# Performance work log

Hardware: AMD Instinct MI355X
Metric: run time of the kernel (lower is better)

Reference implementation:

```python
import jax, jax.numpy as jnp
import numpy as np

TEMP = 0.5
EPS = 1e-12  # matches torch F.normalize default eps


def _l2_normalize(x):
    n = jnp.sqrt(jnp.sum(x * x, axis=1, keepdims=True))
    return x / jnp.maximum(n, EPS)


def setup_inputs() -> dict:
    key = jax.random.key(0)
    k1, k2 = jax.random.split(key)
    B, D = 4096, 256
    return {
        "x_i": jax.random.normal(k1, (B, D), dtype=jnp.float32),
        "x_j": jax.random.normal(k2, (B, D), dtype=jnp.float32),
    }


def reference(x_i, x_j):
    B = x_i.shape[0]
    z = jnp.concatenate([_l2_normalize(x_i), _l2_normalize(x_j)], axis=0)  # [2B, D]
    # cosine similarity of normalized vectors == plain matmul
    sim = z @ z.T  # [2B, 2B]
    pos = jnp.concatenate([jnp.diagonal(sim, B), jnp.diagonal(sim, -B)], axis=0)  # [2B]
    neg_mask = 1.0 - jnp.eye(2 * B, dtype=sim.dtype)
    denom = jnp.sum(neg_mask * jnp.exp(sim / TEMP), axis=1)  # [2B]
    # -log(exp(pos/T) / denom) = -pos/T + log(denom)
    loss = jnp.sum(-(pos / TEMP) + jnp.log(denom)) / (2 * B)
    return loss
```

## Files before the change

kernel.cpp:

```cpp
#include <hip/hip_runtime.h>
#include <hip/hip_bf16.h>

#define B_ROWS 4096
#define NROWS  8192
#define D      256
#define TILES  64
#define NPAIRS 2080

typedef __attribute__((ext_vector_type(8))) short bf16x8;
typedef __attribute__((ext_vector_type(4))) float floatx4;

__device__ __forceinline__ void load16_to_lds(const short* g, short* l) {
    __builtin_amdgcn_global_load_lds(
        (const __attribute__((address_space(1))) unsigned int*)g,
        (__attribute__((address_space(3))) unsigned int*)l,
        16, 0, 0);
}

__global__ __launch_bounds__(256) void norm_pos_kernel(
    const float* __restrict__ xi, const float* __restrict__ xj,
    short* __restrict__ z, float* __restrict__ pos,
    float* __restrict__ selfdot) {
    int p    = blockIdx.x * 4 + (threadIdx.x >> 6);
    int lane = threadIdx.x & 63;
    float4 v1 = ((const float4*)(xi + (size_t)p * D))[lane];
    float4 v2 = ((const float4*)(xj + (size_t)p * D))[lane];
    float ss1 = v1.x * v1.x + v1.y * v1.y + v1.z * v1.z + v1.w * v1.w;
    float ss2 = v2.x * v2.x + v2.y * v2.y + v2.z * v2.z + v2.w * v2.w;
#pragma unroll
    for (int off = 32; off > 0; off >>= 1) {
        ss1 += __shfl_xor(ss1, off);
        ss2 += __shfl_xor(ss2, off);
    }
    float sc1 = 1.0f / fmaxf(sqrtf(ss1), 1e-12f);
    float sc2 = 1.0f / fmaxf(sqrtf(ss2), 1e-12f);

    union { __hip_bfloat16 h[4]; short4 s4; } u1, u2;
    u1.h[0] = __float2bfloat16(v1.x * sc1); u1.h[1] = __float2bfloat16(v1.y * sc1);
    u1.h[2] = __float2bfloat16(v1.z * sc1); u1.h[3] = __float2bfloat16(v1.w * sc1);
    u2.h[0] = __float2bfloat16(v2.x * sc2); u2.h[1] = __float2bfloat16(v2.y * sc2);
    u2.h[2] = __float2bfloat16(v2.z * sc2); u2.h[3] = __float2bfloat16(v2.w * sc2);
    ((short4*)(z + (size_t)p * D))[lane]            = u1.s4;
    ((short4*)(z + (size_t)(p + B_ROWS) * D))[lane] = u2.s4;

    float sd1 = 0.f, sd2 = 0.f, dp = 0.f;
#pragma unroll
    for (int j = 0; j < 4; j++) {
        float a = __bfloat162float(u1.h[j]);
        float b = __bfloat162float(u2.h[j]);
        sd1 += a * a; sd2 += b * b; dp += a * b;
    }
#pragma unroll
    for (int off = 32; off > 0; off >>= 1) {
        sd1 += __shfl_xor(sd1, off);
        sd2 += __shfl_xor(sd2, off);
        dp  += __shfl_xor(dp,  off);
    }
    if (lane == 0) {
        pos[p] = dp; pos[p + B_ROWS] = dp;
        selfdot[p] = sd1; selfdot[p + B_ROWS] = sd2;
    }
}

__global__ __launch_bounds__(256) void sim_rowsum_kernel(
    const short* __restrict__ z, float* __restrict__ rowsum) {
    __shared__ short As[4096];
    __shared__ short Bs[4096];
    __shared__ float rs_lds[128];
    __shared__ float cs_lds[128];

    int tid  = threadIdx.x;
    int lane = tid & 63;
    int w    = tid >> 6;
    int lm   = lane & 15;
    int lg   = lane >> 4;

    int bid = blockIdx.x;
    int ti  = (int)((129.0 - sqrt(16641.0 - 8.0 * (double)bid)) * 0.5);
    while (ti > 0 && ti * TILES - ti * (ti - 1) / 2 > bid) ti--;
    while ((ti + 1) * TILES - (ti + 1) * ti / 2 <= bid) ti++;
    int tj = ti + (bid - (ti * TILES - ti * (ti - 1) / 2));
    int m0 = ti * 128, n0 = tj * 128;

    int wr = (w & 1) * 64;
    int wc = (w >> 1) * 64;

    if (tid < 128) { rs_lds[tid] = 0.f; cs_lds[tid] = 0.f; }

    floatx4 acc[4][4];
#pragma unroll
    for (int mi = 0; mi < 4; mi++)
#pragma unroll
        for (int ni = 0; ni < 4; ni++) acc[mi][ni] = (floatx4){0.f, 0.f, 0.f, 0.f};

    for (int k0 = 0; k0 < D; k0 += 32) {
        __syncthreads();
#pragma unroll
        for (int c = 0; c < 2; c++) {
            int r = c * 64 + lane;
            load16_to_lds(z + (size_t)(m0 + r) * D + k0 + w * 8,
                          As + (w * 128 + c * 64) * 8);
            load16_to_lds(z + (size_t)(n0 + r) * D + k0 + w * 8,
                          Bs + (w * 128 + c * 64) * 8);
        }
        __syncthreads();

        bf16x8 a[4], b[4];
#pragma unroll
        for (int mi = 0; mi < 4; mi++)
            a[mi] = *(const bf16x8*)(As + (lg * 128 + wr + mi * 16 + lm) * 8);
#pragma unroll
        for (int ni = 0; ni < 4; ni++)
            b[ni] = *(const bf16x8*)(Bs + (lg * 128 + wc + ni * 16 + lm) * 8);
#pragma unroll
        for (int mi = 0; mi < 4; mi++)
#pragma unroll
            for (int ni = 0; ni < 4; ni++)
                acc[mi][ni] = __builtin_amdgcn_mfma_f32_16x16x32_bf16(
                    a[mi], b[ni], acc[mi][ni], 0, 0, 0);
    }

    float rs[4][4];
    float cs[4];
#pragma unroll
    for (int mi = 0; mi < 4; mi++)
#pragma unroll
        for (int r = 0; r < 4; r++) rs[mi][r] = 0.f;
#pragma unroll
    for (int ni = 0; ni < 4; ni++) cs[ni] = 0.f;

#pragma unroll
    for (int mi = 0; mi < 4; mi++)
#pragma unroll
        for (int ni = 0; ni < 4; ni++)
#pragma unroll
            for (int r = 0; r < 4; r++) {
                float e = __expf(2.0f * acc[mi][ni][r]);
                rs[mi][r] += e;
                cs[ni]    += e;
            }

    bool offdiag = (ti != tj);
#pragma unroll
    for (int mi = 0; mi < 4; mi++)
#pragma unroll
        for (int r = 0; r < 4; r++) {
            float s = rs[mi][r];
            s += __shfl_xor(s, 1); s += __shfl_xor(s, 2);
            s += __shfl_xor(s, 4); s += __shfl_xor(s, 8);
            if (lm == 0) atomicAdd(&rs_lds[wr + mi * 16 + lg * 4 + r], s);
        }
    if (offdiag) {
#pragma unroll
        for (int ni = 0; ni < 4; ni++) {
            float s = cs[ni];
            s += __shfl_xor(s, 16); s += __shfl_xor(s, 32);
            if (lane < 16) atomicAdd(&cs_lds[wc + ni * 16 + lm], s);
        }
    }
    __syncthreads();
    if (tid < 128) {
        atomicAdd(&rowsum[m0 + tid], rs_lds[tid]);
    } else if (offdiag) {
        atomicAdd(&rowsum[n0 + tid - 128], cs_lds[tid - 128]);
    }
}

__global__ void loss_kernel(const float* __restrict__ rowsum,
                            const float* __restrict__ pos,
                            const float* __restrict__ selfdot,
                            float* __restrict__ out) {
    int tid   = threadIdx.x;
    float acc = 0.f;
    for (int r = tid; r < NROWS; r += 256) {
        float denom = rowsum[r] - __expf(2.0f * selfdot[r]);
        acc += -2.0f * pos[r] + logf(denom);
    }
#pragma unroll
    for (int off = 32; off > 0; off >>= 1) acc += __shfl_xor(acc, off);
    __shared__ float sdata[4];
    int lane = tid & 63, w = tid >> 6;
    if (lane == 0) sdata[w] = acc;
    __syncthreads();
    if (tid == 0) {
        float t = sdata[0] + sdata[1] + sdata[2] + sdata[3];
        out[0]  = t / (float)NROWS;
    }
}

extern "C" void kernel_launch(void* const* d_in, const int* in_sizes, int n_in,
                              void* d_out, int out_size, void* d_ws, size_t ws_size,
                              hipStream_t stream) {
    const float* xi = (const float*)d_in[0];
    const float* xj = (const float*)d_in[1];
    float* out      = (float*)d_out;

    char* ws       = (char*)d_ws;
    short* z       = (short*)ws;
    float* rowsum  = (float*)(ws + (size_t)NROWS * D * 2);
    float* pos     = rowsum + NROWS;
    float* selfdot = pos + NROWS;

    hipMemsetAsync(rowsum, 0, NROWS * sizeof(float), stream);
    norm_pos_kernel<<<B_ROWS / 4, 256, 0, stream>>>(xi, xj, z, pos, selfdot);
    sim_rowsum_kernel<<<NPAIRS, 256, 0, stream>>>(z, rowsum);
    loss_kernel<<<1, 256, 0, stream>>>(rowsum, pos, selfdot, out);
}
```

Before: 121.8 us.

## Double-buffer LDS tiles with swizzle, fold memset, parallelize loss reduction

The GEMM tile loop now double-buffers the A/B tiles in LDS, issuing the next k-slice's global-to-LDS loads before computing on the current one, and uses one barrier per iteration instead of two. The LDS layout changes to row-major 32-element rows with an XOR swizzle on the 16-byte chunk index, meant to cut bank conflicts on the MFMA operand reads. The hipMemsetAsync of rowsum is folded into the normalization kernel, which also zeroes the output. The single-block loss kernel becomes a 32-block kernel that combines partial sums with an atomicAdd. The cost is double the LDS per block and a non-deterministic float summation order in the final loss.

```diff
diff --git a/kernel.cpp b/kernel.cpp
--- a/kernel.cpp
+++ b/kernel.cpp
@@ -6,6 +6,7 @@
 #define D      256
 #define TILES  64
 #define NPAIRS 2080
+#define KC     32
 
 typedef __attribute__((ext_vector_type(8))) short bf16x8;
 typedef __attribute__((ext_vector_type(4))) float floatx4;
@@ -20,7 +21,12 @@
 __global__ __launch_bounds__(256) void norm_pos_kernel(
     const float* __restrict__ xi, const float* __restrict__ xj,
     short* __restrict__ z, float* __restrict__ pos,
-    float* __restrict__ selfdot) {
+    float* __restrict__ selfdot, float* __restrict__ rowsum,
+    float* __restrict__ out) {
+    int gt = blockIdx.x * 256 + threadIdx.x;
+    if (gt < NROWS) rowsum[gt] = 0.f;
+    if (gt == 0)    out[0]     = 0.f;
+
     int p    = blockIdx.x * 4 + (threadIdx.x >> 6);
     int lane = threadIdx.x & 63;
     float4 v1 = ((const float4*)(xi + (size_t)p * D))[lane];
@@ -64,8 +70,8 @@
 
 __global__ __launch_bounds__(256) void sim_rowsum_kernel(
     const short* __restrict__ z, float* __restrict__ rowsum) {
-    __shared__ short As[4096];
-    __shared__ short Bs[4096];
+    __shared__ short As[2][4096];
+    __shared__ short Bs[2][4096];
     __shared__ float rs_lds[128];
     __shared__ float cs_lds[128];
 
@@ -87,37 +93,54 @@
 
     if (tid < 128) { rs_lds[tid] = 0.f; cs_lds[tid] = 0.f; }
 
+    int srow = lane >> 2;
+    int scc  = (lane & 3) ^ (srow & 3);
+
     floatx4 acc[4][4];
 #pragma unroll
     for (int mi = 0; mi < 4; mi++)
 #pragma unroll
         for (int ni = 0; ni < 4; ni++) acc[mi][ni] = (floatx4){0.f, 0.f, 0.f, 0.f};
 
-    for (int k0 = 0; k0 < D; k0 += 32) {
-        __syncthreads();
-#pragma unroll
-        for (int c = 0; c < 2; c++) {
-            int r = c * 64 + lane;
-            load16_to_lds(z + (size_t)(m0 + r) * D + k0 + w * 8,
-                          As + (w * 128 + c * 64) * 8);
-            load16_to_lds(z + (size_t)(n0 + r) * D + k0 + w * 8,
-                          Bs + (w * 128 + c * 64) * 8);
-        }
-        __syncthreads();
+    auto stage = [&](int buf, int k0) {
+#pragma unroll
+        for (int h = 0; h < 2; h++) {
+            int r0  = w * 32 + h * 16;
+            int row = r0 + srow;
+            load16_to_lds(z + (size_t)(m0 + row) * D + k0 + scc * 8,
+                          &As[buf][r0 * 32]);
+            load16_to_lds(z + (size_t)(n0 + row) * D + k0 + scc * 8,
+                          &Bs[buf][r0 * 32]);
+        }
+    };
+
+    stage(0, 0);
+    __syncthreads();
+
+#pragma unroll
+    for (int it = 0; it < 8; it++) {
+        int buf = it & 1;
+        if (it < 7) stage(buf ^ 1, (it + 1) * KC);
 
         bf16x8 a[4], b[4];
 #pragma unroll
-        for (int mi = 0; mi < 4; mi++)
-            a[mi] = *(const bf16x8*)(As + (lg * 128 + wr + mi * 16 + lm) * 8);
-#pragma unroll
-        for (int ni = 0; ni < 4; ni++)
-            b[ni] = *(const bf16x8*)(Bs + (lg * 128 + wc + ni * 16 + lm) * 8);
+        for (int mi = 0; mi < 4; mi++) {
+            int row = wr + mi * 16 + lm;
+            a[mi] = *(const bf16x8*)(&As[buf][row * 32 + ((lg ^ (lm & 3)) * 8)]);
+        }
+#pragma unroll
+        for (int ni = 0; ni < 4; ni++) {
+            int row = wc + ni * 16 + lm;
+            b[ni] = *(const bf16x8*)(&Bs[buf][row * 32 + ((lg ^ (lm & 3)) * 8)]);
+        }
 #pragma unroll
         for (int mi = 0; mi < 4; mi++)
 #pragma unroll
             for (int ni = 0; ni < 4; ni++)
                 acc[mi][ni] = __builtin_amdgcn_mfma_f32_16x16x32_bf16(
                     a[mi], b[ni], acc[mi][ni], 0, 0, 0);
+
+        __syncthreads();
     }
 
     float rs[4][4];
@@ -166,25 +189,21 @@
     }
 }
 
-__global__ void loss_kernel(const float* __restrict__ rowsum,
-                            const float* __restrict__ pos,
-                            const float* __restrict__ selfdot,
-                            float* __restrict__ out) {
-    int tid   = threadIdx.x;
-    float acc = 0.f;
-    for (int r = tid; r < NROWS; r += 256) {
-        float denom = rowsum[r] - __expf(2.0f * selfdot[r]);
-        acc += -2.0f * pos[r] + logf(denom);
-    }
-#pragma unroll
-    for (int off = 32; off > 0; off >>= 1) acc += __shfl_xor(acc, off);
+__global__ __launch_bounds__(256) void loss_kernel(
+    const float* __restrict__ rowsum, const float* __restrict__ pos,
+    const float* __restrict__ selfdot, float* __restrict__ out) {
+    int r = blockIdx.x * 256 + threadIdx.x;
+    float denom = rowsum[r] - __expf(2.0f * selfdot[r]);
+    float v = -2.0f * pos[r] + logf(denom);
+#pragma unroll
+    for (int off = 32; off > 0; off >>= 1) v += __shfl_xor(v, off);
     __shared__ float sdata[4];
-    int lane = tid & 63, w = tid >> 6;
-    if (lane == 0) sdata[w] = acc;
+    int lane = threadIdx.x & 63, w = threadIdx.x >> 6;
+    if (lane == 0) sdata[w] = v;
     __syncthreads();
-    if (tid == 0) {
+    if (threadIdx.x == 0) {
         float t = sdata[0] + sdata[1] + sdata[2] + sdata[3];
-        out[0]  = t / (float)NROWS;
+        atomicAdd(out, t / (float)NROWS);
     }
 }
 
@@ -201,8 +220,8 @@
     float* pos     = rowsum + NROWS;
     float* selfdot = pos + NROWS;
 
-    hipMemsetAsync(rowsum, 0, NROWS * sizeof(float), stream);
-    norm_pos_kernel<<<B_ROWS / 4, 256, 0, stream>>>(xi, xj, z, pos, selfdot);
+    norm_pos_kernel<<<B_ROWS / 4, 256, 0, stream>>>(xi, xj, z, pos, selfdot,
+                                                    rowsum, out);
     sim_rowsum_kernel<<<NPAIRS, 256, 0, stream>>>(z, rowsum);
-    loss_kernel<<<1, 256, 0, stream>>>(rowsum, pos, selfdot, out);
-}
+    loss_kernel<<<NROWS / 256, 256, 0, stream>>>(rowsum, pos, selfdot, out);
+}
```

Measured after the change: 106.4 us. 12.7% less time.
